# Performance work log

Measured on AMD Instinct MI355X. Metric: run time of the kernel, lower is better.

Reference implementation:

```python
import jax, jax.numpy as jnp
import numpy as np

B, C, H, W = 32, 17, 96, 72
K = 3
DIL = 1
PAD = (K // 2) * DIL
KK = K * K


def setup_inputs() -> dict:
    key = jax.random.key(0)
    k1, k2, k3, k4, k5 = jax.random.split(key, 5)
    x = jax.random.normal(k1, (B, C, H, W), jnp.float32)
    offsets = jax.random.normal(k2, (B, 2 * C * KK, H, W), jnp.float32)
    mask = jax.random.uniform(k3, (B, C * KK, H, W), jnp.float32)
    # depthwise conv: weight [C_out=C, C_in/groups=1, K, K], bias [C]
    weight = jax.random.normal(k4, (C, 1, K, K), jnp.float32) * 0.1
    bias = jax.random.normal(k5, (C,), jnp.float32) * 0.01
    return {"x": x, "offsets": offsets, "mask": mask, "weight": weight, "bias": bias}


def _deform_conv(x, offsets, mask, weight, bias):
    # Modulated deformable conv (DCNv2), depthwise, offset_groups == channels.
    off = offsets.reshape(B, C, KK, 2, H, W)
    dy = off[:, :, :, 0]  # [B,C,KK,H,W]
    dx = off[:, :, :, 1]
    m = mask.reshape(B, C, KK, H, W)

    ky, kx = jnp.meshgrid(jnp.arange(K), jnp.arange(K), indexing="ij")
    ky = ky.reshape(KK)
    kx = kx.reshape(KK)
    hh = jnp.arange(H)
    ww = jnp.arange(W)
    # base sampling grid [KK,H,W]
    base_y = (-PAD + ky[:, None, None] * DIL + hh[None, :, None] + 0 * ww[None, None, :]).astype(jnp.float32)
    base_x = (-PAD + kx[:, None, None] * DIL + 0 * hh[None, :, None] + ww[None, None, :]).astype(jnp.float32)

    py = base_y[None, None] + dy  # [B,C,KK,H,W]
    px = base_x[None, None] + dx

    y0f = jnp.floor(py)
    x0f = jnp.floor(px)
    wy = py - y0f
    wx = px - x0f
    y0 = y0f.astype(jnp.int32)
    x0 = x0f.astype(jnp.int32)

    img = x.reshape(B, C, H * W)

    def corner(yi, xi, w):
        # zero-padding semantics: out-of-bounds corners contribute 0
        valid = (yi >= 0) & (yi < H) & (xi >= 0) & (xi < W)
        idx = jnp.clip(yi, 0, H - 1) * W + jnp.clip(xi, 0, W - 1)
        v = jnp.take_along_axis(img, idx.reshape(B, C, -1), axis=2).reshape(B, C, KK, H, W)
        return v * jnp.where(valid, w, 0.0)

    val = (corner(y0, x0, (1 - wy) * (1 - wx))
           + corner(y0, x0 + 1, (1 - wy) * wx)
           + corner(y0 + 1, x0, wy * (1 - wx))
           + corner(y0 + 1, x0 + 1, wy * wx))

    out = jnp.einsum("bckhw,ck->bchw", val * m, weight.reshape(C, KK))
    return out + bias[None, :, None, None]


def reference(x, offsets, mask, weight, bias):
    return _deform_conv(x, offsets, mask, weight, bias)
```

## Files before the change

kernel.cpp:

```cpp
#include <hip/hip_runtime.h>

#define Bn   32
#define Cn   17
#define Hn   96
#define Wn   72
#define Kn   3
#define KKn  9
#define PADn 1
#define HWn  (Hn * Wn)
#define TPB  576
#define NPX  4
#define CHUNK (TPB * NPX)
#define NBLK_X (HWn / CHUNK)

#define PSTR 75
#define PROWS 99
#define XS_SIZE (PROWS * PSTR)

typedef float f4 __attribute__((ext_vector_type(4)));

__global__ __launch_bounds__(TPB) void deform_conv_kernel(
    const float* __restrict__ x,
    const float* __restrict__ offsets,
    const float* __restrict__ mask,
    const float* __restrict__ weight,
    const float* __restrict__ bias,
    float* __restrict__ out)
{
    __shared__ float xs[XS_SIZE];

    const int tid = threadIdx.x;
    const int bc  = blockIdx.y;
    const int c   = bc % Cn;

    if (tid < 225) {
        const int r  = (tid < 75) ? 0 : ((tid < 150) ? 97 : 98);
        xs[r * PSTR + (tid % 75)] = 0.f;
    } else if (tid < 513) {
        const int i  = tid - 225;
        const int r  = 1 + i / 3;
        const int j  = i % 3;
        const int cc = (j == 0) ? 0 : (72 + j);
        xs[r * PSTR + cc] = 0.f;
    }

    {
        const f4* __restrict__ xp4 = (const f4*)(x + (size_t)bc * HWn);
        #pragma unroll
        for (int j = 0; j < HWn / 4 / TPB; ++j) {
            const int ci  = j * TPB + tid;
            const f4 v = xp4[ci];
            const int idx = ci * 4;
            const int y = idx / Wn;
            const int xcol = idx - y * Wn;
            float* d = &xs[(y + 1) * PSTR + (xcol + 1)];
            d[0] = v.x; d[1] = v.y; d[2] = v.z; d[3] = v.w;
        }
    }
    __syncthreads();

    const int hw0 = blockIdx.x * CHUNK + tid * NPX;
    const int h   = hw0 / Wn;
    const int w0  = hw0 - h * Wn;

    const float* __restrict__ offp = offsets + (size_t)bc * (KKn * 2 * HWn);
    const float* __restrict__ mp   = mask    + (size_t)bc * (KKn * HWn);
    const float* __restrict__ wp   = weight  + c * KKn;

    const float bv = bias[c];
    float acc[NPX] = {bv, bv, bv, bv};

    const float hf  = (float)h;
    const float wf0 = (float)w0;

    #pragma unroll
    for (int kk = 0; kk < KKn; ++kk) {
        const float wk  = wp[kk];
        const int   ky  = kk / Kn;
        const int   kx  = kk - ky * Kn;
        const float kyo = (float)(ky - PADn);
        const float kxo = (float)(kx - PADn);

        const f4 dy4 = __builtin_nontemporal_load(
            (const f4*)(offp + (size_t)(kk * 2 + 0) * HWn + hw0));
        const f4 dx4 = __builtin_nontemporal_load(
            (const f4*)(offp + (size_t)(kk * 2 + 1) * HWn + hw0));
        const f4 m4  = __builtin_nontemporal_load(
            (const f4*)(mp + (size_t)kk * HWn + hw0));

        const float dyv[NPX] = {dy4.x, dy4.y, dy4.z, dy4.w};
        const float dxv[NPX] = {dx4.x, dx4.y, dx4.z, dx4.w};
        const float mv [NPX] = {m4.x,  m4.y,  m4.z,  m4.w};

        const float hk = hf + kyo;

        #pragma unroll
        for (int p = 0; p < NPX; ++p) {
            float py = hk + dyv[p];
            float px = wf0 + ((float)p + kxo) + dxv[p];
            py = fminf(fmaxf(py, -1.f), (float)Hn);
            px = fminf(fmaxf(px, -1.f), (float)Wn);

            const float y0f = floorf(py);
            const float x0f = floorf(px);
            const float wy  = py - y0f;
            const float wx  = px - x0f;
            const int y0 = (int)y0f;
            const int x0 = (int)x0f;

            const float* pr = &xs[(y0 + 1) * PSTR + (x0 + 1)];
            const float v00 = pr[0];
            const float v01 = pr[1];
            const float v10 = pr[PSTR];
            const float v11 = pr[PSTR + 1];

            const float top = v00 + wx * (v01 - v00);
            const float bot = v10 + wx * (v11 - v10);
            const float v   = top + wy * (bot - top);

            acc[p] += v * (mv[p] * wk);
        }
    }

    f4 o;
    o.x = acc[0]; o.y = acc[1]; o.z = acc[2]; o.w = acc[3];
    __builtin_nontemporal_store(o, (f4*)(out + (size_t)bc * HWn + hw0));
}

extern "C" void kernel_launch(void* const* d_in, const int* in_sizes, int n_in,
                              void* d_out, int out_size, void* d_ws, size_t ws_size,
                              hipStream_t stream) {
    const float* x       = (const float*)d_in[0];
    const float* offsets = (const float*)d_in[1];
    const float* mask    = (const float*)d_in[2];
    const float* weight  = (const float*)d_in[3];
    const float* bias    = (const float*)d_in[4];
    float* out = (float*)d_out;

    dim3 block(TPB, 1, 1);
    dim3 grid(NBLK_X, Bn * Cn, 1);
    deform_conv_kernel<<<grid, block, 0, stream>>>(x, offsets, mask, weight, bias, out);
}
```

Baseline: 440.8 us.

## Shrink blocks to 192 threads and loop each thread over three pixel chunks

```diff
diff --git a/kernel.cpp b/kernel.cpp
--- a/kernel.cpp
+++ b/kernel.cpp
@@ -8,10 +8,12 @@
 #define KKn  9
 #define PADn 1
 #define HWn  (Hn * Wn)
-#define TPB  576
+#define TPB  192
 #define NPX  4
 #define CHUNK (TPB * NPX)
-#define NBLK_X (HWn / CHUNK)
+#define NCHUNK 3
+#define ROWS_PER_BLOCK 32
+#define NBLK_X (Hn / ROWS_PER_BLOCK)
 
 #define PSTR 75
 #define PROWS 99
@@ -19,7 +21,7 @@
 
 typedef float f4 __attribute__((ext_vector_type(4)));
 
-__global__ __launch_bounds__(TPB) void deform_conv_kernel(
+__global__ __launch_bounds__(TPB, 4) void deform_conv_kernel(
     const float* __restrict__ x,
     const float* __restrict__ offsets,
     const float* __restrict__ mask,
@@ -33,14 +35,17 @@
     const int bc  = blockIdx.y;
     const int c   = bc % Cn;
 
-    if (tid < 225) {
-        const int r  = (tid < 75) ? 0 : ((tid < 150) ? 97 : 98);
-        xs[r * PSTR + (tid % 75)] = 0.f;
-    } else if (tid < 513) {
-        const int i  = tid - 225;
-        const int r  = 1 + i / 3;
-        const int j  = i % 3;
-        const int cc = (j == 0) ? 0 : (72 + j);
+    for (int g = tid; g < 513; g += TPB) {
+        int r, cc;
+        if (g < 225) {
+            r  = (g < 75) ? 0 : ((g < 150) ? 97 : 98);
+            cc = g % 75;
+        } else {
+            const int i = g - 225;
+            r  = 1 + i / 3;
+            const int j = i % 3;
+            cc = (j == 0) ? 0 : (72 + j);
+        }
         xs[r * PSTR + cc] = 0.f;
     }
 
@@ -59,72 +64,75 @@
     }
     __syncthreads();
 
-    const int hw0 = blockIdx.x * CHUNK + tid * NPX;
-    const int h   = hw0 / Wn;
-    const int w0  = hw0 - h * Wn;
-
     const float* __restrict__ offp = offsets + (size_t)bc * (KKn * 2 * HWn);
     const float* __restrict__ mp   = mask    + (size_t)bc * (KKn * HWn);
     const float* __restrict__ wp   = weight  + c * KKn;
+    const float bv = bias[c];
+    const size_t ob = (size_t)bc * HWn;
 
-    const float bv = bias[c];
-    float acc[NPX] = {bv, bv, bv, bv};
+    #pragma unroll 1
+    for (int ch = 0; ch < NCHUNK; ++ch) {
+        const int hw0 = blockIdx.x * (CHUNK * NCHUNK) + ch * CHUNK + tid * NPX;
+        const int h   = hw0 / Wn;
+        const int w0  = hw0 - h * Wn;
 
-    const float hf  = (float)h;
-    const float wf0 = (float)w0;
-
-    #pragma unroll
-    for (int kk = 0; kk < KKn; ++kk) {
-        const float wk  = wp[kk];
-        const int   ky  = kk / Kn;
-        const int   kx  = kk - ky * Kn;
-        const float kyo = (float)(ky - PADn);
-        const float kxo = (float)(kx - PADn);
-
-        const f4 dy4 = __builtin_nontemporal_load(
-            (const f4*)(offp + (size_t)(kk * 2 + 0) * HWn + hw0));
-        const f4 dx4 = __builtin_nontemporal_load(
-            (const f4*)(offp + (size_t)(kk * 2 + 1) * HWn + hw0));
-        const f4 m4  = __builtin_nontemporal_load(
-            (const f4*)(mp + (size_t)kk * HWn + hw0));
-
-        const float dyv[NPX] = {dy4.x, dy4.y, dy4.z, dy4.w};
-        const float dxv[NPX] = {dx4.x, dx4.y, dx4.z, dx4.w};
-        const float mv [NPX] = {m4.x,  m4.y,  m4.z,  m4.w};
-
-        const float hk = hf + kyo;
+        float acc[NPX] = {bv, bv, bv, bv};
+        const float hf  = (float)h;
+        const float wf0 = (float)w0;
 
         #pragma unroll
-        for (int p = 0; p < NPX; ++p) {
-            float py = hk + dyv[p];
-            float px = wf0 + ((float)p + kxo) + dxv[p];
-            py = fminf(fmaxf(py, -1.f), (float)Hn);
-            px = fminf(fmaxf(px, -1.f), (float)Wn);
+        for (int kk = 0; kk < KKn; ++kk) {
+            const float wk  = wp[kk];
+            const int   ky  = kk / Kn;
+            const int   kx  = kk - ky * Kn;
+            const float kyo = (float)(ky - PADn);
+            const float kxo = (float)(kx - PADn);
 
-            const float y0f = floorf(py);
-            const float x0f = floorf(px);
-            const float wy  = py - y0f;
-            const float wx  = px - x0f;
-            const int y0 = (int)y0f;
-            const int x0 = (int)x0f;
+            const f4 dy4 = __builtin_nontemporal_load(
+                (const f4*)(offp + (size_t)(kk * 2 + 0) * HWn + hw0));
+            const f4 dx4 = __builtin_nontemporal_load(
+                (const f4*)(offp + (size_t)(kk * 2 + 1) * HWn + hw0));
+            const f4 m4  = __builtin_nontemporal_load(
+                (const f4*)(mp + (size_t)kk * HWn + hw0));
 
-            const float* pr = &xs[(y0 + 1) * PSTR + (x0 + 1)];
-            const float v00 = pr[0];
-            const float v01 = pr[1];
-            const float v10 = pr[PSTR];
-            const float v11 = pr[PSTR + 1];
+            const float dyv[NPX] = {dy4.x, dy4.y, dy4.z, dy4.w};
+            const float dxv[NPX] = {dx4.x, dx4.y, dx4.z, dx4.w};
+            const float mv [NPX] = {m4.x,  m4.y,  m4.z,  m4.w};
 
-            const float top = v00 + wx * (v01 - v00);
-            const float bot = v10 + wx * (v11 - v10);
-            const float v   = top + wy * (bot - top);
+            const float hk = hf + kyo;
 
-            acc[p] += v * (mv[p] * wk);
+            #pragma unroll
+            for (int p = 0; p < NPX; ++p) {
+                float py = hk + dyv[p];
+                float px = wf0 + ((float)p + kxo) + dxv[p];
+                py = fminf(fmaxf(py, -1.f), (float)Hn);
+                px = fminf(fmaxf(px, -1.f), (float)Wn);
+
+                const float y0f = floorf(py);
+                const float x0f = floorf(px);
+                const float wy  = py - y0f;
+                const float wx  = px - x0f;
+                const int y0 = (int)y0f;
+                const int x0 = (int)x0f;
+
+                const float* pr = &xs[(y0 + 1) * PSTR + (x0 + 1)];
+                const float v00 = pr[0];
+                const float v01 = pr[1];
+                const float v10 = pr[PSTR];
+                const float v11 = pr[PSTR + 1];
+
+                const float top = v00 + wx * (v01 - v00);
+                const float bot = v10 + wx * (v11 - v10);
+                const float v   = top + wy * (bot - top);
+
+                acc[p] += v * (mv[p] * wk);
+            }
         }
+
+        f4 o;
+        o.x = acc[0]; o.y = acc[1]; o.z = acc[2]; o.w = acc[3];
+        __builtin_nontemporal_store(o, (f4*)(out + ob + hw0));
     }
-
-    f4 o;
-    o.x = acc[0]; o.y = acc[1]; o.z = acc[2]; o.w = acc[3];
-    __builtin_nontemporal_store(o, (f4*)(out + (size_t)bc * HWn + hw0));
 }
 
 extern "C" void kernel_launch(void* const* d_in, const int* in_sizes, int n_in,
```

Measured after the change: 468.0 us. +6.2%, slower.
